# Optimization experiments

Measured on AMD Instinct MI355X. Metric: run time of the kernel, lower is better.

Reference implementation:

```python
import jax, jax.numpy as jnp
import numpy as np

T = 4            # number of node types (len(output_sizes))
N = 16384        # nodes per type
D_IN = 512       # input_size
D_H = 1024       # hidden_size
OUT_SIZES = (128, 96, 64, 32)
MAX_OUT = max(OUT_SIZES)


def setup_inputs() -> dict:
    key = jax.random.key(0)
    ks = jax.random.split(key, 16)
    inp = {}
    for t in range(T):
        inp[f"x{t}"] = jax.random.normal(ks[t], (N, D_IN), jnp.float32)
    # nodes are grouped by type (sorted), matching the padded dict layout
    inp["node_type"] = jnp.repeat(jnp.arange(T, dtype=jnp.int64), N)
    # layer1: per-type Linear(input_size, hidden_size) (apply_net)
    inp["W1"] = jax.random.normal(ks[4], (T, D_IN, D_H), jnp.float32) * 0.02
    inp["b1"] = jnp.zeros((T, D_H), jnp.float32)
    # layer2: per-type Linear(hidden_size, out_size_t)
    for t in range(T):
        inp[f"W2_{t}"] = jax.random.normal(ks[5 + t], (D_H, OUT_SIZES[t]), jnp.float32) * 0.02
        inp[f"b2_{t}"] = jnp.zeros((OUT_SIZES[t],), jnp.float32)
    return inp


def reference(x0, x1, x2, x3, node_type, W1, b1,
              W2_0, b2_0, W2_1, b2_1, W2_2, b2_2, W2_3, b2_3):
    # Per-type gather is implicit: x{t} already holds the features of the
    # nodes whose node_type == t (node_type is sorted/blocked).
    xs = jnp.stack([x0, x1, x2, x3])                       # [T, N, D_IN]
    # apply_net: layer1 per type + activation (batched grouped-GEMM)
    h = jax.nn.relu(jnp.einsum('tni,tih->tnh', xs, W1) + b1[:, None, :])  # [T, N, D_H]
    W2s = (W2_0, W2_1, W2_2, W2_3)
    b2s = (b2_0, b2_1, b2_2, b2_3)
    outs = []
    for t in range(T):  # fixed small set of structurally distinct heads
        o = h[t] @ W2s[t] + b2s[t]                         # [N, out_t]
        outs.append(jnp.pad(o, ((0, 0), (0, MAX_OUT - o.shape[1]))))  # _pad to MAX_OUT
    return jnp.stack(outs)                                 # [T, N, MAX_OUT]
```

## Files before the change

### kernel.cpp

```cpp
#include <hip/hip_runtime.h>
#include <hip/hip_bf16.h>


typedef __attribute__((ext_vector_type(8))) short short8;
typedef __attribute__((ext_vector_type(4))) float f32x4;

#define NT 4
#define NNODE 16384
#define DIN 512
#define DH 1024
#define MAXO 128

static __device__ __forceinline__ ushort f2bf(float f) {
    __hip_bfloat16 h = __float2bfloat16(f);
    return *reinterpret_cast<ushort*>(&h);
}

#define GLD(gsrc, ldst)                                                        \
    __builtin_amdgcn_global_load_lds(                                          \
        (const __attribute__((address_space(1))) void*)(gsrc),                 \
        (__attribute__((address_space(3))) void*)(ldst), 16, 0, 0)

__global__ __launch_bounds__(256) void cvt_x_kernel(
    const float* __restrict__ x0, const float* __restrict__ x1,
    const float* __restrict__ x2, const float* __restrict__ x3,
    ushort* __restrict__ out) {
    const int i = blockIdx.x * 256 + threadIdx.x;
    const int per_t = (NNODE * DIN) / 8;
    const int t = i >> 20;
    const int loc = i & (per_t - 1);
    const float* x = (t == 0) ? x0 : (t == 1) ? x1 : (t == 2) ? x2 : x3;
    const float4* xv = reinterpret_cast<const float4*>(x) + (size_t)loc * 2;
    float4 a = xv[0], b = xv[1];
    union { short8 v; ushort u[8]; } r;
    float f[8] = {a.x, a.y, a.z, a.w, b.x, b.y, b.z, b.w};
#pragma unroll
    for (int j = 0; j < 8; ++j) r.u[j] = f2bf(f[j]);
    reinterpret_cast<short8*>(out)[i] = r.v;
}

__global__ __launch_bounds__(256) void cvt_w_t_kernel(
    const float* __restrict__ in, ushort* __restrict__ out,
    int R, int Cin, size_t in_tstride, size_t out_tstride) {
    __shared__ float tile[32][33];
    const int t = blockIdx.z;
    in += (size_t)t * in_tstride;
    out += (size_t)t * out_tstride;
    const int c0 = blockIdx.x * 32, r0 = blockIdx.y * 32;
    const int cx = threadIdx.x & 31;
    const int ry = threadIdx.x >> 5;
#pragma unroll
    for (int j = 0; j < 4; ++j) {
        int rr = ry + j * 8;
        int c = c0 + cx;
        tile[rr][cx] = (c < Cin) ? in[(size_t)(r0 + rr) * Cin + c] : 0.0f;
    }
    __syncthreads();
#pragma unroll
    for (int j = 0; j < 4; ++j) {
        int cc = ry + j * 8;
        out[(size_t)(c0 + cc) * R + r0 + cx] = f2bf(tile[cx][cc]);
    }
}

__global__ void pad_b2_kernel(const float* __restrict__ b0, const float* __restrict__ b1,
                              const float* __restrict__ b2, const float* __restrict__ b3,
                              float* __restrict__ out) {
    const int i = threadIdx.x;
    const int t = i >> 7, n = i & 127;
    const int sz[4] = {128, 96, 64, 32};
    const float* b = (t == 0) ? b0 : (t == 1) ? b1 : (t == 2) ? b2 : b3;
    out[i] = (n < sz[t]) ? b[n] : 0.0f;
}

template <int BN, bool RELU, bool OUTBF16>
__global__ __launch_bounds__(512, 1) void gemm8p(
    const ushort* __restrict__ Abase, const ushort* __restrict__ Bbase,
    const float* __restrict__ biasbase, void* __restrict__ Cbase,
    int M, int N, int K, int MT,
    size_t strideA, size_t strideB, size_t strideBias, size_t strideC) {
    constexpr int NF = BN / 64;
    constexpr int NBU = BN / 128;
    constexpr int ABYTES = 256 * 64 * 2;
    constexpr int BBYTES = BN * 64 * 2;
    constexpr int BUFBYTES = ABYTES + BBYTES;
    __shared__ char lds[2 * BUFBYTES];

    const int cpx = gridDim.x >> 3;
    const int g = blockIdx.x;
    const int wg = (g & 7) * cpx + (g >> 3);
    const int NTL = N / BN;
    const int t = wg / (MT * NTL);
    const int rmn = wg % (MT * NTL);
    const int m0 = (rmn / NTL) * 256;
    const int n0 = (rmn % NTL) * BN;

    const ushort* A = Abase + (size_t)t * strideA;
    const ushort* Bp = Bbase + (size_t)t * strideB;
    const float* bias = biasbase + (size_t)t * strideBias;

    const int tid = threadIdx.x;
    const int lane = tid & 63;
    const int w = tid >> 6;
    const int wm = w >> 2, wn = w & 3;
    const int lrow = lane & 15, lgrp = lane >> 4;

    const ushort* asrc[2][2];
    const ushort* bsrc[2][2];
    int adst[2][2], bdst[2][2];
#pragma unroll
    for (int j = 0; j < 2; ++j) {
        const int cc = j * 512 + tid;
        const int lr = cc >> 3;
        const int cbs = ((cc & 7) * 16) ^ ((lr & 7) << 4);
#pragma unroll
        for (int u = 0; u < 2; ++u) {
            asrc[u][j] = A + (size_t)(m0 + (lr >> 6) * 128 + u * 64 + (lr & 63)) * K
                           + (cbs >> 1);
            adst[u][j] = u * 16384 + cc * 16;
        }
#pragma unroll
        for (int u = 0; u < NBU; ++u) {
            bsrc[u][j] = Bp + (size_t)(n0 + u * 128 + lr) * K + (cbs >> 1);
            bdst[u][j] = ABYTES + u * 16384 + cc * 16;
        }
    }

    f32x4 acc[8][NF] = {};

    const int NK = K / 64;

#pragma unroll
    for (int u = 0; u < NBU; ++u) {
        GLD(bsrc[u][0], lds + bdst[u][0]);
        GLD(bsrc[u][1], lds + bdst[u][1]);
    }
#pragma unroll
    for (int u = 0; u < 2; ++u) {
        GLD(asrc[u][0], lds + adst[u][0]);
        GLD(asrc[u][1], lds + adst[u][1]);
    }
    asm volatile("s_waitcnt vmcnt(0)" ::: "memory");
    __builtin_amdgcn_s_barrier();

    for (int i = 0; i < NK; ++i) {
        const int cur = i & 1;
        const int nxtoff = (cur ^ 1) * BUFBYTES;
        const int ktn = (i + 1 < NK) ? (i + 1) * 64 : 0;
        const char* Al = lds + cur * BUFBYTES;
        const char* Bl = Al + ABYTES;
#pragma unroll
        for (int q = 0; q < 4; ++q) {
            short8 af[2][2], bfr[NF][2];
#pragma unroll
            for (int kkk = 0; kkk < 2; ++kkk) {
#pragma unroll
                for (int ml = 0; ml < 2; ++ml) {
                    const int lr = wm * 64 + (q & 1) * 32 + ml * 16 + lrow;
                    const int row = (q >> 1) * 128 + lr;
                    const int kb = (kkk * 64 + lgrp * 16) ^ ((lr & 7) << 4);
                    af[ml][kkk] = *(const short8*)(Al + row * 128 + kb);
                }
#pragma unroll
                for (int ni = 0; ni < NF; ++ni) {
                    const int br = wn * (NF * 16) + ni * 16 + lrow;
                    const int kb = (kkk * 64 + lgrp * 16) ^ ((br & 7) << 4);
                    bfr[ni][kkk] = *(const short8*)(Bl + br * 128 + kb);
                }
            }
            if (q < NBU) {
                GLD(bsrc[q][0] + ktn, lds + nxtoff + bdst[q][0]);
                GLD(bsrc[q][1] + ktn, lds + nxtoff + bdst[q][1]);
            } else if (q < NBU + 2) {
                constexpr int off = 0;
                const int u = q - NBU;
                if (u == 0) {
                    GLD(asrc[0][0] + ktn, lds + nxtoff + adst[0][0]);
                    GLD(asrc[0][1] + ktn, lds + nxtoff + adst[0][1]);
                } else {
                    GLD(asrc[1][0] + ktn, lds + nxtoff + adst[1][0]);
                    GLD(asrc[1][1] + ktn, lds + nxtoff + adst[1][1]);
                }
                (void)off;
            }
            asm volatile("" ::: "memory");
            __builtin_amdgcn_s_barrier();
            __builtin_amdgcn_sched_barrier(0);
            __builtin_amdgcn_s_setprio(1);
#pragma unroll
            for (int kkk = 0; kkk < 2; ++kkk)
#pragma unroll
                for (int ml = 0; ml < 2; ++ml)
#pragma unroll
                    for (int ni = 0; ni < NF; ++ni)
                        acc[q * 2 + ml][ni] = __builtin_amdgcn_mfma_f32_16x16x32_bf16(
                            af[ml][kkk], bfr[ni][kkk], acc[q * 2 + ml][ni], 0, 0, 0);
            __builtin_amdgcn_s_setprio(0);
            if (q == 1) asm volatile("s_waitcnt vmcnt(4)" ::: "memory");
            if (q == 3) asm volatile("s_waitcnt vmcnt(2)" ::: "memory");
            asm volatile("" ::: "memory");
            __builtin_amdgcn_s_barrier();
        }
    }

    const int wnoff = n0 + wn * (NF * 16);
    const int wmoff = m0 + wm * 128;
#pragma unroll
    for (int ni = 0; ni < NF; ++ni) {
        const int col = wnoff + ni * 16 + lrow;
        const float bv = bias[col];
#pragma unroll
        for (int mi = 0; mi < 8; ++mi) {
            const int row = wmoff + mi * 16 + lgrp * 4;
#pragma unroll
            for (int r = 0; r < 4; ++r) {
                float v = acc[mi][ni][r] + bv;
                if (RELU) v = fmaxf(v, 0.0f);
                if (OUTBF16) {
                    ((ushort*)Cbase)[(size_t)t * strideC + (size_t)(row + r) * N + col] =
                        f2bf(v);
                } else {
                    ((float*)Cbase)[(size_t)t * strideC + (size_t)(row + r) * N + col] = v;
                }
            }
        }
    }
}

extern "C" void kernel_launch(void* const* d_in, const int* in_sizes, int n_in,
                              void* d_out, int out_size, void* d_ws, size_t ws_size,
                              hipStream_t stream) {
    const float* x0 = (const float*)d_in[0];
    const float* x1 = (const float*)d_in[1];
    const float* x2 = (const float*)d_in[2];
    const float* x3 = (const float*)d_in[3];
    const float* W1 = (const float*)d_in[5];
    const float* b1 = (const float*)d_in[6];
    const float* W2[4] = {(const float*)d_in[7], (const float*)d_in[9],
                          (const float*)d_in[11], (const float*)d_in[13]};
    const float* b2[4] = {(const float*)d_in[8], (const float*)d_in[10],
                          (const float*)d_in[12], (const float*)d_in[14]};

    char* ws = (char*)d_ws;
    ushort* H   = (ushort*)ws;
    ushort* Xbf = (ushort*)(ws + 134217728ull);
    ushort* W1T = (ushort*)(ws + 134217728ull + 67108864ull);
    ushort* W2T = (ushort*)(ws + 134217728ull + 67108864ull + 4194304ull);
    float*  b2p = (float*)(ws + 134217728ull + 67108864ull + 4194304ull + 1048576ull);

    cvt_x_kernel<<<16384, 256, 0, stream>>>(x0, x1, x2, x3, Xbf);
    cvt_w_t_kernel<<<dim3(32, 16, 4), 256, 0, stream>>>(
        W1, W1T, DIN, DH, (size_t)DIN * DH, (size_t)DH * DIN);
    const int osz[4] = {128, 96, 64, 32};
    for (int t = 0; t < 4; ++t)
        cvt_w_t_kernel<<<dim3(4, 32, 1), 256, 0, stream>>>(
            W2[t], W2T + (size_t)t * MAXO * DH, DH, osz[t], 0, 0);
    pad_b2_kernel<<<1, 512, 0, stream>>>(b2[0], b2[1], b2[2], b2[3], b2p);

    gemm8p<256, true, true><<<1024, 512, 0, stream>>>(
        Xbf, W1T, b1, H,
        NNODE, DH, DIN, NNODE / 256,
        (size_t)NNODE * DIN, (size_t)DH * DIN, (size_t)DH, (size_t)NNODE * DH);

    gemm8p<128, false, false><<<256, 512, 0, stream>>>(
        H, W2T, b2p, d_out,
        NNODE, MAXO, DH, NNODE / 256,
        (size_t)NNODE * DH, (size_t)MAXO * DH, (size_t)MAXO, (size_t)NNODE * MAXO);
}
```

Before: 190.7 us.

## Hoist B fragment loads out of q loop and restripe A tile LDS layout

The B-operand LDS fragments are now loaded once per K step at q==0 and reused across all four q sub-steps, where before they were reloaded every sub-step. The A tile is reorganised into four 32-row stripes of 8KB each, loaded with one 16-byte global-to-LDS copy per thread per stripe, and the warp-to-row mapping changes to match. On the final iteration the redundant prefetch is skipped and the wait counts are adjusted. This cuts LDS read traffic at the cost of holding B fragments in registers across the whole K step.

```diff
diff --git a/kernel.cpp b/kernel.cpp
--- a/kernel.cpp
+++ b/kernel.cpp
@@ -105,29 +105,31 @@
     const int wm = w >> 2, wn = w & 3;
     const int lrow = lane & 15, lgrp = lane >> 4;
 
-    const ushort* asrc[2][2];
-    const ushort* bsrc[2][2];
-    int adst[2][2], bdst[2][2];
+    const ushort* asrc[4];
+    {
+        const int lr = tid >> 3, c8 = tid & 7;
+        const int cbs = (c8 * 16) ^ ((lr & 7) << 4);
+#pragma unroll
+        for (int u = 0; u < 4; ++u)
+            asrc[u] = A + (size_t)(m0 + (lr >> 5) * 128 + u * 32 + (lr & 31)) * K
+                        + (cbs >> 1);
+    }
+    const ushort* bsrc[NBU][2];
+    int bdst[NBU][2];
 #pragma unroll
     for (int j = 0; j < 2; ++j) {
         const int cc = j * 512 + tid;
         const int lr = cc >> 3;
         const int cbs = ((cc & 7) * 16) ^ ((lr & 7) << 4);
 #pragma unroll
-        for (int u = 0; u < 2; ++u) {
-            asrc[u][j] = A + (size_t)(m0 + (lr >> 6) * 128 + u * 64 + (lr & 63)) * K
-                           + (cbs >> 1);
-            adst[u][j] = u * 16384 + cc * 16;
-        }
-#pragma unroll
         for (int u = 0; u < NBU; ++u) {
             bsrc[u][j] = Bp + (size_t)(n0 + u * 128 + lr) * K + (cbs >> 1);
             bdst[u][j] = ABYTES + u * 16384 + cc * 16;
         }
     }
+    const int adst = tid * 16;
 
     f32x4 acc[8][NF] = {};
-
     const int NK = K / 64;
 
 #pragma unroll
@@ -136,52 +138,57 @@
         GLD(bsrc[u][1], lds + bdst[u][1]);
     }
 #pragma unroll
-    for (int u = 0; u < 2; ++u) {
-        GLD(asrc[u][0], lds + adst[u][0]);
-        GLD(asrc[u][1], lds + adst[u][1]);
-    }
+    for (int u = 0; u < 4; ++u) GLD(asrc[u], lds + u * 8192 + adst);
     asm volatile("s_waitcnt vmcnt(0)" ::: "memory");
     __builtin_amdgcn_s_barrier();
 
     for (int i = 0; i < NK; ++i) {
         const int cur = i & 1;
         const int nxtoff = (cur ^ 1) * BUFBYTES;
-        const int ktn = (i + 1 < NK) ? (i + 1) * 64 : 0;
+        const int ktn = (i + 1) * 64;
+        const bool st = (i + 1 < NK);
         const char* Al = lds + cur * BUFBYTES;
         const char* Bl = Al + ABYTES;
+        short8 bfr[NF][2];
 #pragma unroll
         for (int q = 0; q < 4; ++q) {
-            short8 af[2][2], bfr[NF][2];
-#pragma unroll
-            for (int kkk = 0; kkk < 2; ++kkk) {
+            if (q == 0) {
+#pragma unroll
+                for (int kkk = 0; kkk < 2; ++kkk)
+#pragma unroll
+                    for (int ni = 0; ni < NF; ++ni) {
+                        const int br = wn * (NF * 16) + ni * 16 + lrow;
+                        const int kb = (kkk * 64 + lgrp * 16) ^ ((br & 7) << 4);
+                        bfr[ni][kkk] = *(const short8*)(Bl + br * 128 + kb);
+                    }
+            }
+            short8 af[2][2];
+#pragma unroll
+            for (int kkk = 0; kkk < 2; ++kkk)
 #pragma unroll
                 for (int ml = 0; ml < 2; ++ml) {
-                    const int lr = wm * 64 + (q & 1) * 32 + ml * 16 + lrow;
-                    const int row = (q >> 1) * 128 + lr;
+                    const int lr = wm * 32 + ml * 16 + lrow;
                     const int kb = (kkk * 64 + lgrp * 16) ^ ((lr & 7) << 4);
-                    af[ml][kkk] = *(const short8*)(Al + row * 128 + kb);
+                    af[ml][kkk] = *(const short8*)(Al + q * 8192 + lr * 128 + kb);
                 }
-#pragma unroll
-                for (int ni = 0; ni < NF; ++ni) {
-                    const int br = wn * (NF * 16) + ni * 16 + lrow;
-                    const int kb = (kkk * 64 + lgrp * 16) ^ ((br & 7) << 4);
-                    bfr[ni][kkk] = *(const short8*)(Bl + br * 128 + kb);
+            if (st) {
+                if constexpr (NBU == 2) {
+                    if (q == 0) { GLD(bsrc[0][0] + ktn, lds + nxtoff + bdst[0][0]);
+                                  GLD(bsrc[0][1] + ktn, lds + nxtoff + bdst[0][1]); }
+                    if (q == 1) { GLD(bsrc[1][0] + ktn, lds + nxtoff + bdst[1][0]);
+                                  GLD(bsrc[1][1] + ktn, lds + nxtoff + bdst[1][1]); }
+                    if (q == 2) { GLD(asrc[0] + ktn, lds + nxtoff + adst);
+                                  GLD(asrc[1] + ktn, lds + nxtoff + 8192 + adst); }
+                    if (q == 3) { GLD(asrc[2] + ktn, lds + nxtoff + 16384 + adst);
+                                  GLD(asrc[3] + ktn, lds + nxtoff + 24576 + adst); }
+                } else {
+                    if (q == 0) { GLD(bsrc[0][0] + ktn, lds + nxtoff + bdst[0][0]);
+                                  GLD(bsrc[0][1] + ktn, lds + nxtoff + bdst[0][1]); }
+                    if (q == 1) { GLD(asrc[0] + ktn, lds + nxtoff + adst);
+                                  GLD(asrc[1] + ktn, lds + nxtoff + 8192 + adst); }
+                    if (q == 2) { GLD(asrc[2] + ktn, lds + nxtoff + 16384 + adst);
+                                  GLD(asrc[3] + ktn, lds + nxtoff + 24576 + adst); }
                 }
-            }
-            if (q < NBU) {
-                GLD(bsrc[q][0] + ktn, lds + nxtoff + bdst[q][0]);
-                GLD(bsrc[q][1] + ktn, lds + nxtoff + bdst[q][1]);
-            } else if (q < NBU + 2) {
-                constexpr int off = 0;
-                const int u = q - NBU;
-                if (u == 0) {
-                    GLD(asrc[0][0] + ktn, lds + nxtoff + adst[0][0]);
-                    GLD(asrc[0][1] + ktn, lds + nxtoff + adst[0][1]);
-                } else {
-                    GLD(asrc[1][0] + ktn, lds + nxtoff + adst[1][0]);
-                    GLD(asrc[1][1] + ktn, lds + nxtoff + adst[1][1]);
-                }
-                (void)off;
             }
             asm volatile("" ::: "memory");
             __builtin_amdgcn_s_barrier();
@@ -196,8 +203,11 @@
                         acc[q * 2 + ml][ni] = __builtin_amdgcn_mfma_f32_16x16x32_bf16(
                             af[ml][kkk], bfr[ni][kkk], acc[q * 2 + ml][ni], 0, 0, 0);
             __builtin_amdgcn_s_setprio(0);
-            if (q == 1) asm volatile("s_waitcnt vmcnt(4)" ::: "memory");
-            if (q == 3) asm volatile("s_waitcnt vmcnt(2)" ::: "memory");
+            if (q == 1) {
+                if (st) asm volatile("s_waitcnt vmcnt(4)" ::: "memory");
+                else    asm volatile("s_waitcnt vmcnt(0)" ::: "memory");
+            }
+            if (q == 3 && st) asm volatile("s_waitcnt vmcnt(2)" ::: "memory");
             asm volatile("" ::: "memory");
             __builtin_amdgcn_s_barrier();
         }
```

Result: faster. 184.6 us (-3.2%).

## Restructure GEMM K-loop into two phases with swapped MFMA operands and vector stores

Applied to the files above, without the earlier changes.

Replaces the four-quarter inner schedule with two phases per K step. Each phase loads B fragments once and four A fragments, so B is reused across both halves. MFMA operands are swapped so each lane holds four consecutive columns of one row, which enables float4 bias loads and packed vector stores in the epilogue. Prefetch of the next tile is skipped on the last iteration instead of reloading tile zero. The change cuts LDS reads and barriers per K step and widens global stores, at the cost of more fragment registers held live and a different vmcnt wait schedule.

```diff
diff --git a/kernel.cpp b/kernel.cpp
--- a/kernel.cpp
+++ b/kernel.cpp
@@ -74,7 +74,7 @@
 }
 
 template <int BN, bool RELU, bool OUTBF16>
-__global__ __launch_bounds__(512, 1) void gemm8p(
+__global__ __launch_bounds__(512, 1) void gemm2p(
     const ushort* __restrict__ Abase, const ushort* __restrict__ Bbase,
     const float* __restrict__ biasbase, void* __restrict__ Cbase,
     int M, int N, int K, int MT,
@@ -106,8 +106,8 @@
     const int lrow = lane & 15, lgrp = lane >> 4;
 
     const ushort* asrc[2][2];
-    const ushort* bsrc[2][2];
-    int adst[2][2], bdst[2][2];
+    const ushort* bsrc[NBU][2];
+    int adst[2][2], bdst[NBU][2];
 #pragma unroll
     for (int j = 0; j < 2; ++j) {
         const int cc = j * 512 + tid;
@@ -127,7 +127,6 @@
     }
 
     f32x4 acc[8][NF] = {};
-
     const int NK = K / 64;
 
 #pragma unroll
@@ -146,42 +145,36 @@
     for (int i = 0; i < NK; ++i) {
         const int cur = i & 1;
         const int nxtoff = (cur ^ 1) * BUFBYTES;
-        const int ktn = (i + 1 < NK) ? (i + 1) * 64 : 0;
+        const int ktn = (i + 1) * 64;
+        const bool st = (i + 1 < NK);
         const char* Al = lds + cur * BUFBYTES;
         const char* Bl = Al + ABYTES;
-#pragma unroll
-        for (int q = 0; q < 4; ++q) {
-            short8 af[2][2], bfr[NF][2];
-#pragma unroll
-            for (int kkk = 0; kkk < 2; ++kkk) {
-#pragma unroll
-                for (int ml = 0; ml < 2; ++ml) {
-                    const int lr = wm * 64 + (q & 1) * 32 + ml * 16 + lrow;
-                    const int row = (q >> 1) * 128 + lr;
-                    const int kb = (kkk * 64 + lgrp * 16) ^ ((lr & 7) << 4);
-                    af[ml][kkk] = *(const short8*)(Al + row * 128 + kb);
-                }
+        short8 bfr[NF][2];
+
+        {
+#pragma unroll
+            for (int kkk = 0; kkk < 2; ++kkk)
 #pragma unroll
                 for (int ni = 0; ni < NF; ++ni) {
                     const int br = wn * (NF * 16) + ni * 16 + lrow;
                     const int kb = (kkk * 64 + lgrp * 16) ^ ((br & 7) << 4);
                     bfr[ni][kkk] = *(const short8*)(Bl + br * 128 + kb);
                 }
-            }
-            if (q < NBU) {
-                GLD(bsrc[q][0] + ktn, lds + nxtoff + bdst[q][0]);
-                GLD(bsrc[q][1] + ktn, lds + nxtoff + bdst[q][1]);
-            } else if (q < NBU + 2) {
-                constexpr int off = 0;
-                const int u = q - NBU;
-                if (u == 0) {
-                    GLD(asrc[0][0] + ktn, lds + nxtoff + adst[0][0]);
-                    GLD(asrc[0][1] + ktn, lds + nxtoff + adst[0][1]);
-                } else {
-                    GLD(asrc[1][0] + ktn, lds + nxtoff + adst[1][0]);
-                    GLD(asrc[1][1] + ktn, lds + nxtoff + adst[1][1]);
+            short8 af[4][2];
+#pragma unroll
+            for (int kkk = 0; kkk < 2; ++kkk)
+#pragma unroll
+                for (int ml = 0; ml < 4; ++ml) {
+                    const int lr = wm * 64 + ml * 16 + lrow;
+                    const int kb = (kkk * 64 + lgrp * 16) ^ ((lr & 7) << 4);
+                    af[ml][kkk] = *(const short8*)(Al + lr * 128 + kb);
                 }
-                (void)off;
+            if (st) {
+#pragma unroll
+                for (int u = 0; u < NBU; ++u) {
+                    GLD(bsrc[u][0] + ktn, lds + nxtoff + bdst[u][0]);
+                    GLD(bsrc[u][1] + ktn, lds + nxtoff + bdst[u][1]);
+                }
             }
             asm volatile("" ::: "memory");
             __builtin_amdgcn_s_barrier();
@@ -190,38 +183,85 @@
 #pragma unroll
             for (int kkk = 0; kkk < 2; ++kkk)
 #pragma unroll
-                for (int ml = 0; ml < 2; ++ml)
+                for (int ml = 0; ml < 4; ++ml)
 #pragma unroll
                     for (int ni = 0; ni < NF; ++ni)
-                        acc[q * 2 + ml][ni] = __builtin_amdgcn_mfma_f32_16x16x32_bf16(
-                            af[ml][kkk], bfr[ni][kkk], acc[q * 2 + ml][ni], 0, 0, 0);
+                        acc[ml][ni] = __builtin_amdgcn_mfma_f32_16x16x32_bf16(
+                            bfr[ni][kkk], af[ml][kkk], acc[ml][ni], 0, 0, 0);
             __builtin_amdgcn_s_setprio(0);
-            if (q == 1) asm volatile("s_waitcnt vmcnt(4)" ::: "memory");
-            if (q == 3) asm volatile("s_waitcnt vmcnt(2)" ::: "memory");
+            if (st) {
+                if constexpr (NBU == 2)
+                    asm volatile("s_waitcnt vmcnt(4)" ::: "memory");
+                else
+                    asm volatile("s_waitcnt vmcnt(2)" ::: "memory");
+            } else {
+                asm volatile("s_waitcnt vmcnt(0)" ::: "memory");
+            }
             asm volatile("" ::: "memory");
             __builtin_amdgcn_s_barrier();
         }
+
+        {
+            short8 af[4][2];
+#pragma unroll
+            for (int kkk = 0; kkk < 2; ++kkk)
+#pragma unroll
+                for (int ml = 0; ml < 4; ++ml) {
+                    const int lr = wm * 64 + ml * 16 + lrow;
+                    const int kb = (kkk * 64 + lgrp * 16) ^ ((lr & 7) << 4);
+                    af[ml][kkk] = *(const short8*)(Al + 16384 + lr * 128 + kb);
+                }
+            if (st) {
+                GLD(asrc[0][0] + ktn, lds + nxtoff + adst[0][0]);
+                GLD(asrc[0][1] + ktn, lds + nxtoff + adst[0][1]);
+                GLD(asrc[1][0] + ktn, lds + nxtoff + adst[1][0]);
+                GLD(asrc[1][1] + ktn, lds + nxtoff + adst[1][1]);
+            }
+            asm volatile("" ::: "memory");
+            __builtin_amdgcn_s_barrier();
+            __builtin_amdgcn_sched_barrier(0);
+            __builtin_amdgcn_s_setprio(1);
+#pragma unroll
+            for (int kkk = 0; kkk < 2; ++kkk)
+#pragma unroll
+                for (int ml = 0; ml < 4; ++ml)
+#pragma unroll
+                    for (int ni = 0; ni < NF; ++ni)
+                        acc[4 + ml][ni] = __builtin_amdgcn_mfma_f32_16x16x32_bf16(
+                            bfr[ni][kkk], af[ml][kkk], acc[4 + ml][ni], 0, 0, 0);
+            __builtin_amdgcn_s_setprio(0);
+            if (st) asm volatile("s_waitcnt vmcnt(2)" ::: "memory");
+            asm volatile("" ::: "memory");
+            __builtin_amdgcn_s_barrier();
+        }
     }
 
     const int wnoff = n0 + wn * (NF * 16);
     const int wmoff = m0 + wm * 128;
 #pragma unroll
     for (int ni = 0; ni < NF; ++ni) {
-        const int col = wnoff + ni * 16 + lrow;
-        const float bv = bias[col];
+        const int ncol = wnoff + ni * 16 + lgrp * 4;
+        const float4 bv = *reinterpret_cast<const float4*>(&bias[ncol]);
 #pragma unroll
         for (int mi = 0; mi < 8; ++mi) {
-            const int row = wmoff + mi * 16 + lgrp * 4;
-#pragma unroll
-            for (int r = 0; r < 4; ++r) {
-                float v = acc[mi][ni][r] + bv;
-                if (RELU) v = fmaxf(v, 0.0f);
-                if (OUTBF16) {
-                    ((ushort*)Cbase)[(size_t)t * strideC + (size_t)(row + r) * N + col] =
-                        f2bf(v);
-                } else {
-                    ((float*)Cbase)[(size_t)t * strideC + (size_t)(row + r) * N + col] = v;
-                }
+            const int row = wmoff + mi * 16 + lrow;
+            float v0 = acc[mi][ni][0] + bv.x;
+            float v1 = acc[mi][ni][1] + bv.y;
+            float v2 = acc[mi][ni][2] + bv.z;
+            float v3 = acc[mi][ni][3] + bv.w;
+            if (RELU) {
+                v0 = fmaxf(v0, 0.0f); v1 = fmaxf(v1, 0.0f);
+                v2 = fmaxf(v2, 0.0f); v3 = fmaxf(v3, 0.0f);
+            }
+            const size_t base = (size_t)t * strideC + (size_t)row * N + ncol;
+            if (OUTBF16) {
+                uint2 p;
+                p.x = (uint)f2bf(v0) | ((uint)f2bf(v1) << 16);
+                p.y = (uint)f2bf(v2) | ((uint)f2bf(v3) << 16);
+                *reinterpret_cast<uint2*>(&((ushort*)Cbase)[base]) = p;
+            } else {
+                float4 p = {v0, v1, v2, v3};
+                *reinterpret_cast<float4*>(&((float*)Cbase)[base]) = p;
             }
         }
     }
@@ -257,12 +297,12 @@
             W2[t], W2T + (size_t)t * MAXO * DH, DH, osz[t], 0, 0);
     pad_b2_kernel<<<1, 512, 0, stream>>>(b2[0], b2[1], b2[2], b2[3], b2p);
 
-    gemm8p<256, true, true><<<1024, 512, 0, stream>>>(
+    gemm2p<256, true, true><<<1024, 512, 0, stream>>>(
         Xbf, W1T, b1, H,
         NNODE, DH, DIN, NNODE / 256,
         (size_t)NNODE * DIN, (size_t)DH * DIN, (size_t)DH, (size_t)NNODE * DH);
 
-    gemm8p<128, false, false><<<256, 512, 0, stream>>>(
+    gemm2p<128, false, false><<<256, 512, 0, stream>>>(
         H, W2T, b2p, d_out,
         NNODE, MAXO, DH, NNODE / 256,
         (size_t)NNODE * DH, (size_t)MAXO * DH, (size_t)MAXO, (size_t)NNODE * MAXO);
```

New measurement: 179.3 us. 1.06x faster.
